# Kernel tuning notes

Measured on AMD Instinct MI355X. Metric: run time of the kernel, lower is better.

## Reference

```python
import jax, jax.numpy as jnp
import numpy as np

HEADS = 4
DIM_HEAD = 128


def setup_inputs() -> dict:
    key = jax.random.key(0)
    k1, k2, k3, k4 = jax.random.split(key, 4)
    B, C, H, W = 8, 256, 64, 64
    hidden = HEADS * DIM_HEAD  # 512
    x = jax.random.normal(k1, (B, C, H, W), dtype=jnp.float32)
    # 1x1 convs are just channel matmuls; store kernels as [out_ch, in_ch]
    w_qkv = jax.random.normal(k2, (3 * hidden, C), dtype=jnp.float32) * 0.05
    w_out = jax.random.normal(k3, (C, hidden), dtype=jnp.float32) * 0.05
    b_out = jax.random.normal(k4, (C,), dtype=jnp.float32) * 0.05
    return {"x": x, "w_qkv": w_qkv, "w_out": w_out, "b_out": b_out}


def reference(x, w_qkv, w_out, b_out):
    B, C, H, W = x.shape
    n = H * W
    # to_qkv: 1x1 conv without bias == channel matmul
    qkv = jnp.einsum('bchw,oc->bohw', x, w_qkv)  # [B, 3*heads*dim_head, H, W]
    qkv = qkv.reshape(B, 3, HEADS, DIM_HEAD, n)  # 'b (qkv heads c) h w -> b qkv heads c n'
    q, k, v = qkv[:, 0], qkv[:, 1], qkv[:, 2]    # each [B, heads, dim_head, n]
    k = jax.nn.softmax(k, axis=-1)               # softmax over spatial positions
    context = jnp.einsum('bhdn,bhen->bhde', k, v)   # [B, heads, d, e]
    out = jnp.einsum('bhde,bhdn->bhen', context, q)  # [B, heads, e, n]
    out = out.reshape(B, HEADS * DIM_HEAD, H, W)
    # to_out: 1x1 conv with bias
    return jnp.einsum('bchw,oc->bohw', out, w_out) + b_out[None, :, None, None]
```

## Files before the change

kernel.cpp:

```cpp
#include <hip/hip_runtime.h>
#include <stdint.h>


using frag8 = __attribute__((ext_vector_type(8))) short;
using f32x4 = __attribute__((ext_vector_type(4))) float;

__device__ __forceinline__ float bf2f(unsigned short u) {
    union { unsigned int u; float f; } c;
    c.u = ((unsigned int)u) << 16;
    return c.f;
}
__device__ __forceinline__ unsigned short f2bf(float f) {
    union { float f; unsigned int u; } c; c.f = f;
    unsigned int u = c.u;
    return (unsigned short)((u + 0x7FFFu + ((u >> 16) & 1u)) >> 16);
}

__device__ __forceinline__ void gl_lds16(const void* g, void* l) {
    __builtin_amdgcn_global_load_lds(
        (const __attribute__((address_space(1))) unsigned int*)g,
        (__attribute__((address_space(3))) unsigned int*)l, 16, 0, 0);
}

__global__ __launch_bounds__(256) void k0_weights(
    const float* __restrict__ w_qkv, const float* __restrict__ w_out,
    unsigned short* __restrict__ wkvb, unsigned short* __restrict__ woutb,
    unsigned short* __restrict__ wqT)
{
    __shared__ float T[64][65];
    const int blk = blockIdx.x;
    const int tid = threadIdx.x;
    if (blk < 256) {
        const int idx = (blk * 256 + tid) * 4;
        float4 v = *(const float4*)(w_qkv + 512 * 256 + idx);
        ushort4 o;
        o.x = f2bf(v.x); o.y = f2bf(v.y); o.z = f2bf(v.z); o.w = f2bf(v.w);
        *(ushort4*)(wkvb + idx) = o;
    } else if (blk < 384) {
        const int idx = ((blk - 256) * 256 + tid) * 4;
        float4 v = *(const float4*)(w_out + idx);
        ushort4 o;
        o.x = f2bf(v.x); o.y = f2bf(v.y); o.z = f2bf(v.z); o.w = f2bf(v.w);
        *(ushort4*)(woutb + idx) = o;
    } else {
        const int t = blk - 384;
        const int j0 = (t >> 2) * 64, c0 = (t & 3) * 64;
        const int r = tid >> 4, cc = (tid & 15) * 4;
        #pragma unroll
        for (int p = 0; p < 4; ++p) {
            float4 v = *(const float4*)(w_qkv + (j0 + r + p * 16) * 256 + c0 + cc);
            T[r + p * 16][cc + 0] = v.x; T[r + p * 16][cc + 1] = v.y;
            T[r + p * 16][cc + 2] = v.z; T[r + p * 16][cc + 3] = v.w;
        }
        __syncthreads();
        const int c = tid >> 2, jj = (tid & 3) * 16;
        #pragma unroll
        for (int g = 0; g < 4; ++g) {
            ushort4 o;
            o.x = f2bf(T[jj + g * 4 + 0][c]);
            o.y = f2bf(T[jj + g * 4 + 1][c]);
            o.z = f2bf(T[jj + g * 4 + 2][c]);
            o.w = f2bf(T[jj + g * 4 + 3][c]);
            *(ushort4*)(wqT + (c0 + c) * 512 + j0 + jj + g * 4) = o;
        }
    }
}

__global__ __launch_bounds__(256) void k0_xt(
    const float* __restrict__ x, unsigned short* __restrict__ xbT)
{
    __shared__ float T[64][65];
    const int tid = threadIdx.x;
    const int n0 = blockIdx.x * 64, c0 = blockIdx.y * 64, b = blockIdx.z;
    const float* xb = x + (size_t)b * 1048576;
    const int cr = tid >> 4, nc = (tid & 15) * 4;
    #pragma unroll
    for (int p = 0; p < 4; ++p) {
        float4 v = *(const float4*)(xb + (size_t)(c0 + cr + p * 16) * 4096 + n0 + nc);
        T[cr + p * 16][nc + 0] = v.x; T[cr + p * 16][nc + 1] = v.y;
        T[cr + p * 16][nc + 2] = v.z; T[cr + p * 16][nc + 3] = v.w;
    }
    __syncthreads();
    const int n = tid >> 2, cc = (tid & 3) * 16;
    unsigned short* dst = xbT + (size_t)b * 1048576 + (size_t)(n0 + n) * 256 + c0 + cc;
    #pragma unroll
    for (int g = 0; g < 4; ++g) {
        ushort4 o;
        o.x = f2bf(T[cc + g * 4 + 0][n]);
        o.y = f2bf(T[cc + g * 4 + 1][n]);
        o.z = f2bf(T[cc + g * 4 + 2][n]);
        o.w = f2bf(T[cc + g * 4 + 3][n]);
        *(ushort4*)(dst + g * 4) = o;
    }
}

template<int MODE>
__global__ __launch_bounds__(256) void mfma_bt(
    const unsigned short* __restrict__ A0, int lda,
    const unsigned short* __restrict__ B0, int ldb,
    void* __restrict__ C0, int ldc,
    const float* __restrict__ bias, int Kp,
    unsigned long long sAz, unsigned long long sBz, unsigned long long sCz)
{
    __shared__ unsigned short As[128 * 32];
    __shared__ unsigned short Bs[128 * 32];
    const int tid  = threadIdx.x;
    const int w    = tid >> 6, lane = tid & 63;
    const int quad = lane >> 4, l16 = lane & 15;
    const int wm = (w >> 1) * 64, wn = (w & 1) * 64;
    const int z = blockIdx.z;

    const unsigned short* A;
    const unsigned short* B;
    int ks, ke, m0, n0;
    if constexpr (MODE == 2) {
        m0 = 0; n0 = 0;
        ks = blockIdx.x * 512; ke = ks + 512;
        const unsigned long long off =
            ((unsigned long long)(z >> 2) * 1024ull + (unsigned long long)(z & 3) * 128ull) * 4096ull;
        A = A0 + off; B = B0 + off;
    } else if constexpr (MODE == 3) {
        m0 = blockIdx.y * 128; n0 = 0;
        ks = 0; ke = Kp;
        A = A0 + (unsigned long long)(z & 3) * 128ull + (unsigned long long)m0 * lda;
        B = B0 + (unsigned long long)z * 16384ull;
    } else {
        m0 = blockIdx.y * 128; n0 = blockIdx.x * 128;
        ks = 0; ke = Kp;
        A = A0 + sAz * z + (unsigned long long)m0 * lda;
        B = B0 + sBz * z + (unsigned long long)n0 * ldb;
    }

    const int cA0 = w * 128 + lane;
    const int cA1 = cA0 + 64;
    const unsigned short* gA0 = A + (unsigned long long)(cA0 >> 2) * lda + (cA0 & 3) * 8;
    const unsigned short* gA1 = A + (unsigned long long)(cA1 >> 2) * lda + (cA1 & 3) * 8;
    const unsigned short* gB0 = B + (unsigned long long)(cA0 >> 2) * ldb + (cA0 & 3) * 8;
    const unsigned short* gB1 = B + (unsigned long long)(cA1 >> 2) * ldb + (cA1 & 3) * 8;
    unsigned short* lA0 = As + w * 1024;
    unsigned short* lA1 = As + w * 1024 + 512;
    unsigned short* lB0 = Bs + w * 1024;
    unsigned short* lB1 = Bs + w * 1024 + 512;

    f32x4 acc[4][4] = {};

    for (int k0 = ks; k0 < ke; k0 += 32) {
        gl_lds16(gA0 + k0, lA0);
        gl_lds16(gA1 + k0, lA1);
        gl_lds16(gB0 + k0, lB0);
        gl_lds16(gB1 + k0, lB1);
        __syncthreads();
        frag8 a[4], b[4];
        #pragma unroll
        for (int t = 0; t < 4; ++t) {
            a[t] = *(const frag8*)(As + (wm + t * 16 + l16) * 32 + quad * 8);
            b[t] = *(const frag8*)(Bs + (wn + t * 16 + l16) * 32 + quad * 8);
        }
        #pragma unroll
        for (int mt = 0; mt < 4; ++mt)
            #pragma unroll
            for (int nt = 0; nt < 4; ++nt)
                acc[mt][nt] = __builtin_amdgcn_mfma_f32_16x16x32_bf16(
                    a[mt], b[nt], acc[mt][nt], 0, 0, 0);
        __syncthreads();
    }

    if constexpr (MODE == 0 || MODE == 3) {
        unsigned short* C;
        if constexpr (MODE == 0)
            C = (unsigned short*)C0 + sCz * z + (unsigned long long)m0 * ldc + n0;
        else
            C = (unsigned short*)C0 + (unsigned long long)(z >> 2) * 131072ull
              + (unsigned long long)(z & 3) * 128ull + (unsigned long long)m0 * ldc;
        #pragma unroll
        for (int mt = 0; mt < 4; ++mt) {
            const int row = wm + mt * 16 + quad * 4;
            #pragma unroll
            for (int nt = 0; nt < 4; ++nt) {
                const int col = wn + nt * 16 + l16;
                #pragma unroll
                for (int r = 0; r < 4; ++r)
                    C[(unsigned long long)(row + r) * ldc + col] = f2bf(acc[mt][nt][r]);
            }
        }
    } else if constexpr (MODE == 1) {
        float* C = (float*)C0 + sCz * z + (unsigned long long)m0 * ldc + n0;
        const float* bp = bias + m0;
        #pragma unroll
        for (int mt = 0; mt < 4; ++mt) {
            const int row = wm + mt * 16 + quad * 4;
            #pragma unroll
            for (int nt = 0; nt < 4; ++nt) {
                const int col = wn + nt * 16 + l16;
                #pragma unroll
                for (int r = 0; r < 4; ++r)
                    C[(unsigned long long)(row + r) * ldc + col] = acc[mt][nt][r] + bp[row + r];
            }
        }
    } else {
        float* C = (float*)C0 + ((unsigned long long)blockIdx.x * 32 + z) * 16384ull;
        #pragma unroll
        for (int mt = 0; mt < 4; ++mt) {
            const int row = wm + mt * 16 + quad * 4;
            #pragma unroll
            for (int nt = 0; nt < 4; ++nt) {
                const int col = wn + nt * 16 + l16;
                #pragma unroll
                for (int r = 0; r < 4; ++r)
                    C[(row + r) * 128 + col] = acc[mt][nt][r];
            }
        }
    }
}

__global__ __launch_bounds__(256) void k2_softmax(unsigned short* __restrict__ kv)
{
    __shared__ float red[4];
    const int idx = blockIdx.x;
    const int b = idx >> 9, r = idx & 511;
    unsigned short* row = kv + (size_t)(b * 1024 + r) * 4096;
    const int tid = threadIdx.x;
    float v[16];
    #pragma unroll
    for (int g = 0; g < 4; ++g) {
        ushort4 u = *(const ushort4*)(row + g * 1024 + tid * 4);
        v[g * 4 + 0] = bf2f(u.x); v[g * 4 + 1] = bf2f(u.y);
        v[g * 4 + 2] = bf2f(u.z); v[g * 4 + 3] = bf2f(u.w);
    }
    float m = -1e30f;
    #pragma unroll
    for (int i = 0; i < 16; ++i) m = fmaxf(m, v[i]);
    #pragma unroll
    for (int off = 32; off > 0; off >>= 1) m = fmaxf(m, __shfl_down(m, off, 64));
    if ((tid & 63) == 0) red[tid >> 6] = m;
    __syncthreads();
    m = fmaxf(fmaxf(red[0], red[1]), fmaxf(red[2], red[3]));
    __syncthreads();
    float s = 0.f;
    #pragma unroll
    for (int i = 0; i < 16; ++i) { v[i] = __expf(v[i] - m); s += v[i]; }
    #pragma unroll
    for (int off = 32; off > 0; off >>= 1) s += __shfl_down(s, off, 64);
    if ((tid & 63) == 0) red[tid >> 6] = s;
    __syncthreads();
    s = red[0] + red[1] + red[2] + red[3];
    const float inv = 1.0f / s;
    #pragma unroll
    for (int g = 0; g < 4; ++g) {
        ushort4 u;
        u.x = f2bf(v[g * 4 + 0] * inv); u.y = f2bf(v[g * 4 + 1] * inv);
        u.z = f2bf(v[g * 4 + 2] * inv); u.w = f2bf(v[g * 4 + 3] * inv);
        *(ushort4*)(row + g * 1024 + tid * 4) = u;
    }
}

__global__ __launch_bounds__(256) void k3_sum(
    const float* __restrict__ ctxp, unsigned short* __restrict__ ctxb)
{
    const int idx = (blockIdx.x * 256 + threadIdx.x) * 4;
    float4 s = make_float4(0.f, 0.f, 0.f, 0.f);
    #pragma unroll
    for (int sl = 0; sl < 8; ++sl) {
        float4 t = *(const float4*)(ctxp + (size_t)sl * 524288 + idx);
        s.x += t.x; s.y += t.y; s.z += t.z; s.w += t.w;
    }
    ushort4 o;
    o.x = f2bf(s.x); o.y = f2bf(s.y); o.z = f2bf(s.z); o.w = f2bf(s.w);
    *(ushort4*)(ctxb + idx) = o;
}

extern "C" void kernel_launch(void* const* d_in, const int* in_sizes, int n_in,
                              void* d_out, int out_size, void* d_ws, size_t ws_size,
                              hipStream_t stream) {
    (void)in_sizes; (void)n_in; (void)out_size; (void)ws_size;
    const float* x     = (const float*)d_in[0];
    const float* w_qkv = (const float*)d_in[1];
    const float* w_out = (const float*)d_in[2];
    const float* b_out = (const float*)d_in[3];
    float* out = (float*)d_out;

    char* ws = (char*)d_ws;
    unsigned short* kv    = (unsigned short*)ws;
    unsigned short* xbT   = (unsigned short*)(ws + 67108864);
    unsigned short* wkvb  = (unsigned short*)(ws + 83886080);
    unsigned short* woutb = (unsigned short*)(ws + 84410368);
    unsigned short* wqT   = (unsigned short*)(ws + 84672512);
    float*          ctxp  = (float*)(ws + 84934656);
    unsigned short* ctxb  = (unsigned short*)(ws + 101711872);
    unsigned short* Mb    = (unsigned short*)(ws + 102760448);
    unsigned short* Nb    = (unsigned short*)(ws + 104857600);

    k0_weights<<<dim3(416), 256, 0, stream>>>(w_qkv, w_out, wkvb, woutb, wqT);
    k0_xt<<<dim3(64, 4, 8), 256, 0, stream>>>(x, xbT);
    mfma_bt<0><<<dim3(32, 8, 8), 256, 0, stream>>>(
        wkvb, 256, xbT, 256, kv, 4096, nullptr, 256,
        0ull, 1048576ull, 4194304ull);
    k2_softmax<<<dim3(4096), 256, 0, stream>>>(kv);
    mfma_bt<2><<<dim3(8, 1, 32), 256, 0, stream>>>(
        kv, 4096, kv + (size_t)512 * 4096, 4096, ctxp, 128, nullptr, 0,
        0ull, 0ull, 0ull);
    k3_sum<<<dim3(512), 256, 0, stream>>>(ctxp, ctxb);
    mfma_bt<3><<<dim3(1, 2, 32), 256, 0, stream>>>(
        woutb, 512, ctxb, 128, Mb, 512, nullptr, 128,
        0ull, 0ull, 0ull);
    mfma_bt<0><<<dim3(2, 2, 8), 256, 0, stream>>>(
        Mb, 512, wqT, 512, Nb, 256, nullptr, 512,
        131072ull, 0ull, 65536ull);
    mfma_bt<1><<<dim3(32, 2, 8), 256, 0, stream>>>(
        Nb, 256, xbT, 256, out, 4096, b_out, 256,
        65536ull, 1048576ull, 1048576ull);
}
```

Measured before the change: 184.1 us.

## Fuse K softmax exp into QKV GEMM epilogue and defer normalization

The QKV projection epilogue now computes exp of the K rows directly, stores them as bf16, and atomically accumulates per-row sums. Normalization is deferred to a small scale kernel applied to the context matrix, which removes the separate softmax pass over the K tensor. The split-K context partials are also accumulated with float atomics into one buffer instead of eight slices followed by a reduction, which needs a memset. Dropping max-subtraction risks overflow for large logits, and the atomics make results nondeterministic.

```diff
diff --git a/kernel.cpp b/kernel.cpp
--- a/kernel.cpp
+++ b/kernel.cpp
@@ -183,6 +183,48 @@
                     C[(unsigned long long)(row + r) * ldc + col] = f2bf(acc[mt][nt][r]);
             }
         }
+    } else if constexpr (MODE == 4) {
+        unsigned short* C = (unsigned short*)C0 + sCz * z + (unsigned long long)m0 * ldc + n0;
+        if (blockIdx.y < 4) {
+            float* rs = (float*)bias;
+            #pragma unroll
+            for (int mt = 0; mt < 4; ++mt) {
+                const int row = wm + mt * 16 + quad * 4;
+                float rsum[4] = {0.f, 0.f, 0.f, 0.f};
+                #pragma unroll
+                for (int nt = 0; nt < 4; ++nt) {
+                    const int col = wn + nt * 16 + l16;
+                    #pragma unroll
+                    for (int r = 0; r < 4; ++r) {
+                        float e = __expf(acc[mt][nt][r]);
+                        rsum[r] += e;
+                        C[(unsigned long long)(row + r) * ldc + col] = f2bf(e);
+                    }
+                }
+                #pragma unroll
+                for (int r = 0; r < 4; ++r) {
+                    float v = rsum[r];
+                    v += __shfl_xor(v, 1, 64);
+                    v += __shfl_xor(v, 2, 64);
+                    v += __shfl_xor(v, 4, 64);
+                    v += __shfl_xor(v, 8, 64);
+                    if (l16 == 0)
+                        atomicAdd(rs + (unsigned long long)z * 512 + m0 + row + r, v);
+                }
+            }
+        } else {
+            #pragma unroll
+            for (int mt = 0; mt < 4; ++mt) {
+                const int row = wm + mt * 16 + quad * 4;
+                #pragma unroll
+                for (int nt = 0; nt < 4; ++nt) {
+                    const int col = wn + nt * 16 + l16;
+                    #pragma unroll
+                    for (int r = 0; r < 4; ++r)
+                        C[(unsigned long long)(row + r) * ldc + col] = f2bf(acc[mt][nt][r]);
+                }
+            }
+        }
     } else if constexpr (MODE == 1) {
         float* C = (float*)C0 + sCz * z + (unsigned long long)m0 * ldc + n0;
         const float* bp = bias + m0;
@@ -198,7 +240,7 @@
             }
         }
     } else {
-        float* C = (float*)C0 + ((unsigned long long)blockIdx.x * 32 + z) * 16384ull;
+        float* C = (float*)C0 + (unsigned long long)z * 16384ull;
         #pragma unroll
         for (int mt = 0; mt < 4; ++mt) {
             const int row = wm + mt * 16 + quad * 4;
@@ -207,65 +249,22 @@
                 const int col = wn + nt * 16 + l16;
                 #pragma unroll
                 for (int r = 0; r < 4; ++r)
-                    C[(row + r) * 128 + col] = acc[mt][nt][r];
-            }
-        }
-    }
-}
-
-__global__ __launch_bounds__(256) void k2_softmax(unsigned short* __restrict__ kv)
-{
-    __shared__ float red[4];
-    const int idx = blockIdx.x;
-    const int b = idx >> 9, r = idx & 511;
-    unsigned short* row = kv + (size_t)(b * 1024 + r) * 4096;
-    const int tid = threadIdx.x;
-    float v[16];
-    #pragma unroll
-    for (int g = 0; g < 4; ++g) {
-        ushort4 u = *(const ushort4*)(row + g * 1024 + tid * 4);
-        v[g * 4 + 0] = bf2f(u.x); v[g * 4 + 1] = bf2f(u.y);
-        v[g * 4 + 2] = bf2f(u.z); v[g * 4 + 3] = bf2f(u.w);
-    }
-    float m = -1e30f;
-    #pragma unroll
-    for (int i = 0; i < 16; ++i) m = fmaxf(m, v[i]);
-    #pragma unroll
-    for (int off = 32; off > 0; off >>= 1) m = fmaxf(m, __shfl_down(m, off, 64));
-    if ((tid & 63) == 0) red[tid >> 6] = m;
-    __syncthreads();
-    m = fmaxf(fmaxf(red[0], red[1]), fmaxf(red[2], red[3]));
-    __syncthreads();
-    float s = 0.f;
-    #pragma unroll
-    for (int i = 0; i < 16; ++i) { v[i] = __expf(v[i] - m); s += v[i]; }
-    #pragma unroll
-    for (int off = 32; off > 0; off >>= 1) s += __shfl_down(s, off, 64);
-    if ((tid & 63) == 0) red[tid >> 6] = s;
-    __syncthreads();
-    s = red[0] + red[1] + red[2] + red[3];
-    const float inv = 1.0f / s;
-    #pragma unroll
-    for (int g = 0; g < 4; ++g) {
-        ushort4 u;
-        u.x = f2bf(v[g * 4 + 0] * inv); u.y = f2bf(v[g * 4 + 1] * inv);
-        u.z = f2bf(v[g * 4 + 2] * inv); u.w = f2bf(v[g * 4 + 3] * inv);
-        *(ushort4*)(row + g * 1024 + tid * 4) = u;
-    }
-}
-
-__global__ __launch_bounds__(256) void k3_sum(
-    const float* __restrict__ ctxp, unsigned short* __restrict__ ctxb)
+                    atomicAdd(C + (row + r) * 128 + col, acc[mt][nt][r]);
+            }
+        }
+    }
+}
+
+__global__ __launch_bounds__(256) void k3_scale(
+    const float* __restrict__ ctx, const float* __restrict__ rowsum,
+    unsigned short* __restrict__ ctxb)
 {
     const int idx = (blockIdx.x * 256 + threadIdx.x) * 4;
-    float4 s = make_float4(0.f, 0.f, 0.f, 0.f);
-    #pragma unroll
-    for (int sl = 0; sl < 8; ++sl) {
-        float4 t = *(const float4*)(ctxp + (size_t)sl * 524288 + idx);
-        s.x += t.x; s.y += t.y; s.z += t.z; s.w += t.w;
-    }
+    const float inv = 1.0f / rowsum[idx >> 7];
+    float4 t = *(const float4*)(ctx + idx);
     ushort4 o;
-    o.x = f2bf(s.x); o.y = f2bf(s.y); o.z = f2bf(s.z); o.w = f2bf(s.w);
+    o.x = f2bf(t.x * inv); o.y = f2bf(t.y * inv);
+    o.z = f2bf(t.z * inv); o.w = f2bf(t.w * inv);
     *(ushort4*)(ctxb + idx) = o;
 }
 
@@ -280,26 +279,28 @@
     float* out = (float*)d_out;
 
     char* ws = (char*)d_ws;
-    unsigned short* kv    = (unsigned short*)ws;
-    unsigned short* xbT   = (unsigned short*)(ws + 67108864);
-    unsigned short* wkvb  = (unsigned short*)(ws + 83886080);
-    unsigned short* woutb = (unsigned short*)(ws + 84410368);
-    unsigned short* wqT   = (unsigned short*)(ws + 84672512);
-    float*          ctxp  = (float*)(ws + 84934656);
-    unsigned short* ctxb  = (unsigned short*)(ws + 101711872);
-    unsigned short* Mb    = (unsigned short*)(ws + 102760448);
-    unsigned short* Nb    = (unsigned short*)(ws + 104857600);
+    unsigned short* kv     = (unsigned short*)ws;
+    unsigned short* xbT    = (unsigned short*)(ws + 67108864);
+    unsigned short* wkvb   = (unsigned short*)(ws + 83886080);
+    unsigned short* woutb  = (unsigned short*)(ws + 84410368);
+    unsigned short* wqT    = (unsigned short*)(ws + 84672512);
+    float*          ctx    = (float*)(ws + 84934656);
+    float*          rowsum = (float*)(ws + 87031808);
+    unsigned short* ctxb   = (unsigned short*)(ws + 87048192);
+    unsigned short* Mb     = (unsigned short*)(ws + 88096768);
+    unsigned short* Nb     = (unsigned short*)(ws + 90193920);
+
+    hipMemsetAsync(ws + 84934656, 0, 2097152 + 16384, stream);
 
     k0_weights<<<dim3(416), 256, 0, stream>>>(w_qkv, w_out, wkvb, woutb, wqT);
     k0_xt<<<dim3(64, 4, 8), 256, 0, stream>>>(x, xbT);
-    mfma_bt<0><<<dim3(32, 8, 8), 256, 0, stream>>>(
-        wkvb, 256, xbT, 256, kv, 4096, nullptr, 256,
+    mfma_bt<4><<<dim3(32, 8, 8), 256, 0, stream>>>(
+        wkvb, 256, xbT, 256, kv, 4096, rowsum, 256,
         0ull, 1048576ull, 4194304ull);
-    k2_softmax<<<dim3(4096), 256, 0, stream>>>(kv);
     mfma_bt<2><<<dim3(8, 1, 32), 256, 0, stream>>>(
-        kv, 4096, kv + (size_t)512 * 4096, 4096, ctxp, 128, nullptr, 0,
+        kv, 4096, kv + (size_t)512 * 4096, 4096, ctx, 128, nullptr, 0,
         0ull, 0ull, 0ull);
-    k3_sum<<<dim3(512), 256, 0, stream>>>(ctxp, ctxb);
+    k3_scale<<<dim3(512), 256, 0, stream>>>(ctx, rowsum, ctxb);
     mfma_bt<3><<<dim3(1, 2, 32), 256, 0, stream>>>(
         woutb, 512, ctxb, 128, Mb, 512, nullptr, 128,
         0ull, 0ull, 0ull);
```

Result: slower. 190.9 us (+3.7%).
